# Optimization experiments

Hardware: AMD Instinct MI355X
Metric: run time of the kernel (lower is better)

## Reference

```python
import jax, jax.numpy as jnp
import numpy as np

D_MODEL, D_K, D_V, N_HEADS = 1024, 64, 64, 16


def setup_inputs() -> dict:
    key = jax.random.key(0)
    ks = jax.random.split(key, 8)
    B, S = 2, 2048
    s = 0.02
    return {
        "x": jax.random.normal(ks[0], (B, S, D_MODEL), dtype=jnp.float32),
        "Wq": jax.random.normal(ks[1], (D_MODEL, N_HEADS * D_K), dtype=jnp.float32) * s,
        "bq": jnp.zeros((N_HEADS * D_K,), dtype=jnp.float32),
        "Wk": jax.random.normal(ks[2], (D_MODEL, N_HEADS * D_K), dtype=jnp.float32) * s,
        "bk": jnp.zeros((N_HEADS * D_K,), dtype=jnp.float32),
        "Wv": jax.random.normal(ks[3], (D_MODEL, N_HEADS * D_V), dtype=jnp.float32) * s,
        "bv": jnp.zeros((N_HEADS * D_V,), dtype=jnp.float32),
        "Wo": jax.random.normal(ks[4], (N_HEADS * D_V, D_MODEL), dtype=jnp.float32) * s,
    }


def reference(x, Wq, bq, Wk, bk, Wv, bv, Wo):
    B, S, _ = x.shape
    split = lambda t, d: t.reshape(B, S, N_HEADS, d).transpose(0, 2, 1, 3)  # [B,H,S,d]
    Q = split(x @ Wq + bq, D_K)
    K = split(x @ Wk + bk, D_K)
    V = split(x @ Wv + bv, D_V)
    scores = jnp.einsum("bhqd,bhkd->bhqk", Q / jnp.sqrt(jnp.float32(D_K)), K)
    # causal mask: x + (1 - 1/tril) == 0 on allowed, -inf on disallowed
    causal = jnp.tril(jnp.ones((S, S), dtype=bool))
    scores = jnp.where(causal, scores, -jnp.inf)
    attn = jax.nn.softmax(scores, axis=-1)
    out = jnp.einsum("bhqk,bhkd->bhqd", attn, V)  # [B,H,S,d_v]
    out = out.transpose(0, 2, 1, 3).reshape(B, S, N_HEADS * D_V)
    return out @ Wo
```

## Files before the change

kernel.cpp:

```cpp
#include <hip/hip_runtime.h>
#include <hip/hip_bf16.h>
#include <hip/hip_fp16.h>
#include <cstdint>

#define DEVINL __device__ __forceinline__

typedef __attribute__((ext_vector_type(4))) float floatx4;
typedef __attribute__((ext_vector_type(8))) __bf16 bf16x8;
typedef __attribute__((ext_vector_type(4))) _Float16 half4;
typedef __attribute__((ext_vector_type(8))) _Float16 half8;
typedef __attribute__((ext_vector_type(4))) unsigned short u16x4;

DEVINL floatx4 mfma_16x16x32(bf16x8 a, bf16x8 b, floatx4 c) {
  return __builtin_amdgcn_mfma_f32_16x16x32_bf16(a, b, c, 0, 0, 0);
}
DEVINL floatx4 mfma_16x16x16_f16(half4 a, half4 b, floatx4 c) {
  return __builtin_amdgcn_mfma_f32_16x16x16f16(a, b, c, 0, 0, 0);
}

DEVINL void async_copy16(const void* g, void* l) {
  __builtin_amdgcn_global_load_lds(
      (__attribute__((address_space(1))) void*)(void*)g,
      (__attribute__((address_space(3))) void*)l, 16, 0, 0);
}

#define QSCALE 0.18033688011112042f

#define VS(d, s) \
  ((d) * 128 + (((((s) >> 3)) ^ ((d) & 7)) << 4) + ((s) & 7) * 2)

__global__ void cast_to_bf16(const float* __restrict__ in,
                             __hip_bfloat16* __restrict__ out, int n) {
  int i = (blockIdx.x * blockDim.x + threadIdx.x) * 4;
  if (i + 3 < n) {
    const float4 v = *(const float4*)&in[i];
    out[i + 0] = __float2bfloat16(v.x);
    out[i + 1] = __float2bfloat16(v.y);
    out[i + 2] = __float2bfloat16(v.z);
    out[i + 3] = __float2bfloat16(v.w);
  }
}

__global__ void transpose_cast4(const float* __restrict__ Wq,
                                const float* __restrict__ Wk,
                                const float* __restrict__ Wv,
                                const float* __restrict__ Wo,
                                __hip_bfloat16* __restrict__ Wt,
                                __hip_bfloat16* __restrict__ Wot) {
  __shared__ float tile[32][33];
  const int z = blockIdx.z;
  const float* W = (z == 0) ? Wq : (z == 1) ? Wk : (z == 2) ? Wv : Wo;
  __hip_bfloat16* dst = (z < 3) ? (Wt + ((int64_t)z << 20)) : Wot;
  const int k0 = blockIdx.x * 32, n0 = blockIdx.y * 32;
  const int tx = threadIdx.x, ty = threadIdx.y;
#pragma unroll
  for (int i = 0; i < 32; i += 8)
    tile[ty + i][tx] = W[(int64_t)(k0 + ty + i) * 1024 + n0 + tx];
  __syncthreads();
#pragma unroll
  for (int i = 0; i < 32; i += 8)
    dst[(int64_t)(n0 + ty + i) * 1024 + k0 + tx] =
        __float2bfloat16(tile[tx][ty + i]);
}

template <int MODE>
__global__ __launch_bounds__(256, 2) void gemm_bt(
    const __hip_bfloat16* __restrict__ A, const __hip_bfloat16* __restrict__ Bt,
    int M, int N, int K, const float* __restrict__ bq,
    const float* __restrict__ bk, const float* __restrict__ bv,
    __hip_bfloat16* __restrict__ Qb, __hip_bfloat16* __restrict__ Kb,
    _Float16* __restrict__ Vt, float* __restrict__ outf) {
  __shared__ __align__(16) __hip_bfloat16 As[128 * 32];
  __shared__ __align__(16) __hip_bfloat16 Bs[128 * 32];
  const int tid = threadIdx.x;
  const int wave = tid >> 6, lane = tid & 63;
  const int quad = lane >> 4, l16 = lane & 15;
  const int bm = blockIdx.x * 128, bn = blockIdx.y * 128;
  const int wm = (wave >> 1) * 64, wn = (wave & 1) * 64;

  floatx4 acc[4][4] = {};

  const int arow = tid >> 2, aseg = tid & 3;
  for (int k0 = 0; k0 < K; k0 += 32) {
#pragma unroll
    for (int i = 0; i < 2; ++i) {
      const int row = arow + i * 64;
      const int off = row * 32 + aseg * 8;
      async_copy16(A + (int64_t)(bm + row) * K + k0 + aseg * 8, As + off);
      async_copy16(Bt + (int64_t)(bn + row) * K + k0 + aseg * 8, Bs + off);
    }
    __syncthreads();
    bf16x8 af[4], bfr[4];
#pragma unroll
    for (int i = 0; i < 4; ++i) {
      af[i] = *(const bf16x8*)&As[(wm + i * 16 + l16) * 32 + quad * 8];
      bfr[i] = *(const bf16x8*)&Bs[(wn + i * 16 + l16) * 32 + quad * 8];
    }
#pragma unroll
    for (int i = 0; i < 4; ++i)
#pragma unroll
      for (int j = 0; j < 4; ++j)
        acc[i][j] = mfma_16x16x32(af[i], bfr[j], acc[i][j]);
    __syncthreads();
  }

  if (MODE == 1) {
#pragma unroll
    for (int i = 0; i < 4; ++i)
#pragma unroll
      for (int j = 0; j < 4; ++j) {
        const int n = bn + wn + j * 16 + l16;
#pragma unroll
        for (int r = 0; r < 4; ++r) {
          const int m = bm + wm + i * 16 + quad * 4 + r;
          outf[(int64_t)m * N + n] = acc[i][j][r];
        }
      }
  } else if (bn < 2048) {
#pragma unroll
    for (int i = 0; i < 4; ++i)
#pragma unroll
      for (int j = 0; j < 4; ++j) {
        const int n = bn + wn + j * 16 + l16;
        const int which = n >> 10, nn = n & 1023;
        const int h = nn >> 6, d = nn & 63;
        const float* bias = (which == 0) ? bq : bk;
#pragma unroll
        for (int r = 0; r < 4; ++r) {
          const int m = bm + wm + i * 16 + quad * 4 + r;
          const int b = m >> 11, s = m & 2047;
          float v = acc[i][j][r] + bias[nn];
          if (which == 0) v *= QSCALE;
          ((which == 0) ? Qb : Kb)[((int64_t)(b * 16 + h) * 2048 + s) * 64 + d] =
              __float2bfloat16(v);
        }
      }
  } else {
    char* scr = (wave & 1) ? (char*)Bs : (char*)As;
    const int h = ((bn + wn) & 1023) >> 6;
    const int bb = (bm + wm) >> 11;
    const int sbase = (bm + wm) & 2047;
    _Float16* dstV = Vt + (int64_t)(bb * 16 + h) * 64 * 2048;
#pragma unroll
    for (int phase = 0; phase < 2; ++phase) {
      __syncthreads();
      if ((wave >> 1) == phase) {
#pragma unroll
        for (int i = 0; i < 4; ++i)
#pragma unroll
          for (int j = 0; j < 4; ++j) {
            const int d = j * 16 + l16;
#pragma unroll
            for (int r = 0; r < 4; ++r) {
              const int s = i * 16 + quad * 4 + r;
              *(_Float16*)(scr + VS(d, s)) =
                  (_Float16)(acc[i][j][r] + bv[((bn + wn) & 1023) + d]);
            }
          }
      }
      __syncthreads();
      if ((wave >> 1) == phase) {
#pragma unroll
        for (int it = 0; it < 8; ++it) {
          const int idx = lane + it * 64;
          const int d = idx >> 3, sc = idx & 7;
          const half8 vv =
              *(const half8*)(scr + d * 128 + ((sc ^ (d & 7)) << 4));
          *(half8*)(dstV + (int64_t)d * 2048 + sbase + sc * 8) = vv;
        }
      }
    }
  }
}

__global__ __launch_bounds__(128, 2) void attn_kernel(
    const __hip_bfloat16* __restrict__ Qb, const __hip_bfloat16* __restrict__ Kb,
    const _Float16* __restrict__ Vt, __hip_bfloat16* __restrict__ Ab) {
  __shared__ __align__(16) char smem[32768];
  const int tid = threadIdx.x;
  const int wave = tid >> 6, lane = tid & 63;
  const int quad = lane >> 4, l16 = lane & 15;
  const int c = 31 - (int)(blockIdx.x >> 5);
  const int bh = blockIdx.x & 31;
  const int qbase = c * 64 + wave * 32;
  const int ktmax = c;

  const __hip_bfloat16* Qh = Qb + (int64_t)bh * 2048 * 64;
  const __hip_bfloat16* Kh = Kb + (int64_t)bh * 2048 * 64;
  const _Float16* Vh = Vt + (int64_t)bh * 64 * 2048;

  bf16x8 qf[2][2];
#pragma unroll
  for (int rt = 0; rt < 2; ++rt)
#pragma unroll
    for (int h = 0; h < 2; ++h)
      qf[rt][h] = *(const bf16x8*)&Qh[(int64_t)(qbase + rt * 16 + l16) * 64 +
                                      h * 32 + quad * 8];

  floatx4 o[2][4] = {};
  float lsum[2] = {0.f, 0.f};

  auto stage = [&](int buf, int k0s) {
#pragma unroll
    for (int i = 0; i < 4; ++i) {
      const int p = tid + i * 128;
      const int r = p >> 3, cc = (p & 7) ^ (r & 7);
      async_copy16(Kh + (int64_t)(k0s + r) * 64 + cc * 8,
                   smem + buf * 8192 + p * 16);
      async_copy16(Vh + (int64_t)r * 2048 + k0s + cc * 8,
                   smem + 16384 + buf * 8192 + p * 16);
    }
  };

  stage(0, 0);
  for (int kt = 0; kt <= ktmax; ++kt) {
    const int k0 = kt * 64;
    const int cur = kt & 1;
    __syncthreads();
    if (kt < ktmax) stage(cur ^ 1, k0 + 64);

    const char* kb = smem + cur * 8192;
    const char* vb = smem + 16384 + cur * 8192;
    const int sw = l16 & 7;

    bf16x8 kfr[4][2];
#pragma unroll
    for (int kk = 0; kk < 4; ++kk)
#pragma unroll
      for (int h = 0; h < 2; ++h)
        kfr[kk][h] = *(const bf16x8*)(kb + (kk * 16 + l16) * 128 +
                                      (((h * 4 + quad) ^ sw) << 4));

    floatx4 st[2][4];
#pragma unroll
    for (int kk = 0; kk < 4; ++kk)
#pragma unroll
      for (int rt = 0; rt < 2; ++rt) {
        floatx4 z = {};
        z = mfma_16x16x32(kfr[kk][0], qf[rt][0], z);
        st[rt][kk] = mfma_16x16x32(kfr[kk][1], qf[rt][1], z);
      }

    half4 vfr[4][4];
#pragma unroll
    for (int dt = 0; dt < 4; ++dt)
#pragma unroll
      for (int kk = 0; kk < 4; ++kk)
        vfr[dt][kk] = *(const half4*)(vb + (dt * 16 + l16) * 128 +
                                      (((kk * 2 + (quad >> 1)) ^ sw) << 4) +
                                      (quad & 1) * 8);

    const bool masked = (kt == ktmax);
    half4 pf[2][4];
#pragma unroll
    for (int rt = 0; rt < 2; ++rt) {
      const int qrow = qbase + rt * 16 + l16;
#pragma unroll
      for (int kk = 0; kk < 4; ++kk) {
#pragma unroll
        for (int r = 0; r < 4; ++r) {
          const int key = k0 + kk * 16 + quad * 4 + r;
          float p = __builtin_amdgcn_exp2f(st[rt][kk][r]);
          if (masked && key > qrow) p = 0.f;
          lsum[rt] += p;
          pf[rt][kk][r] = (_Float16)p;
        }
      }
    }

#pragma unroll
    for (int dt = 0; dt < 4; ++dt)
#pragma unroll
      for (int kk = 0; kk < 4; ++kk)
#pragma unroll
        for (int rt = 0; rt < 2; ++rt)
          o[rt][dt] = mfma_16x16x16_f16(vfr[dt][kk], pf[rt][kk], o[rt][dt]);
  }

#pragma unroll
  for (int rt = 0; rt < 2; ++rt) {
    lsum[rt] += __shfl_xor(lsum[rt], 16, 64);
    lsum[rt] += __shfl_xor(lsum[rt], 32, 64);
  }

  const int b = bh >> 4, h = bh & 15;
#pragma unroll
  for (int rt = 0; rt < 2; ++rt) {
    const float invl = 1.0f / lsum[rt];
#pragma unroll
    for (int dt = 0; dt < 4; ++dt) {
      u16x4 pack;
#pragma unroll
      for (int r = 0; r < 4; ++r)
        pack[r] = __builtin_bit_cast(unsigned short,
                                     __float2bfloat16(o[rt][dt][r] * invl));
      *(u16x4*)&Ab[(int64_t)(b * 2048 + qbase + rt * 16 + l16) * 1024 +
                   h * 64 + dt * 16 + quad * 4] = pack;
    }
  }
}

extern "C" void kernel_launch(void* const* d_in, const int* in_sizes, int n_in,
                              void* d_out, int out_size, void* d_ws,
                              size_t ws_size, hipStream_t stream) {
  const float* x = (const float*)d_in[0];
  const float* Wq = (const float*)d_in[1];
  const float* bq = (const float*)d_in[2];
  const float* Wk = (const float*)d_in[3];
  const float* bk = (const float*)d_in[4];
  const float* Wv = (const float*)d_in[5];
  const float* bv = (const float*)d_in[6];
  const float* Wo = (const float*)d_in[7];
  float* out = (float*)d_out;

  char* ws = (char*)d_ws;
  __hip_bfloat16* xb = (__hip_bfloat16*)(ws);
  __hip_bfloat16* Wt = (__hip_bfloat16*)(ws + (8ll << 20));
  __hip_bfloat16* Wot = (__hip_bfloat16*)(ws + (14ll << 20));
  __hip_bfloat16* Qb = (__hip_bfloat16*)(ws + (16ll << 20));
  __hip_bfloat16* Kb = (__hip_bfloat16*)(ws + (24ll << 20));
  _Float16* Vt = (_Float16*)(ws + (32ll << 20));
  __hip_bfloat16* Ab = xb;

  cast_to_bf16<<<4096, 256, 0, stream>>>(x, xb, 4096 * 1024);
  transpose_cast4<<<dim3(32, 32, 4), dim3(32, 8), 0, stream>>>(Wq, Wk, Wv, Wo,
                                                               Wt, Wot);
  gemm_bt<0><<<dim3(32, 24), 256, 0, stream>>>(xb, Wt, 4096, 3072, 1024, bq, bk,
                                               bv, Qb, Kb, Vt, nullptr);
  attn_kernel<<<dim3(1024), 128, 0, stream>>>(Qb, Kb, Vt, Ab);
  gemm_bt<1><<<dim3(32, 8), 256, 0, stream>>>(Ab, Wot, 4096, 1024, 1024,
                                              nullptr, nullptr, nullptr,
                                              nullptr, nullptr, nullptr, out);
}
```

Measured before the change: 182.8 us.

## Fuse prep kernels, widen GEMM K-step to 64 with swizzled LDS, retile output GEMM

```diff
diff --git a/kernel.cpp b/kernel.cpp
--- a/kernel.cpp
+++ b/kernel.cpp
@@ -29,30 +29,33 @@
 #define VS(d, s) \
   ((d) * 128 + (((((s) >> 3)) ^ ((d) & 7)) << 4) + ((s) & 7) * 2)
 
-__global__ void cast_to_bf16(const float* __restrict__ in,
-                             __hip_bfloat16* __restrict__ out, int n) {
-  int i = (blockIdx.x * blockDim.x + threadIdx.x) * 4;
-  if (i + 3 < n) {
-    const float4 v = *(const float4*)&in[i];
-    out[i + 0] = __float2bfloat16(v.x);
-    out[i + 1] = __float2bfloat16(v.y);
-    out[i + 2] = __float2bfloat16(v.z);
-    out[i + 3] = __float2bfloat16(v.w);
-  }
-}
-
-__global__ void transpose_cast4(const float* __restrict__ Wq,
-                                const float* __restrict__ Wk,
-                                const float* __restrict__ Wv,
-                                const float* __restrict__ Wo,
-                                __hip_bfloat16* __restrict__ Wt,
-                                __hip_bfloat16* __restrict__ Wot) {
+__global__ void prep(const float* __restrict__ x, const float* __restrict__ Wq,
+                     const float* __restrict__ Wk, const float* __restrict__ Wv,
+                     const float* __restrict__ Wo,
+                     __hip_bfloat16* __restrict__ xb,
+                     __hip_bfloat16* __restrict__ Wt,
+                     __hip_bfloat16* __restrict__ Wot) {
+  const int z = blockIdx.z;
+  const int tx = threadIdx.x, ty = threadIdx.y;
+  if (z == 4) {
+    const int bi = blockIdx.y * 32 + blockIdx.x;
+    const int tid = ty * 32 + tx;
+    const int base = bi * 4096 + tid * 4;
+#pragma unroll
+    for (int j = 0; j < 4; ++j) {
+      const int i = base + j * 1024;
+      const float4 v = *(const float4*)&x[i];
+      xb[i + 0] = __float2bfloat16(v.x);
+      xb[i + 1] = __float2bfloat16(v.y);
+      xb[i + 2] = __float2bfloat16(v.z);
+      xb[i + 3] = __float2bfloat16(v.w);
+    }
+    return;
+  }
   __shared__ float tile[32][33];
-  const int z = blockIdx.z;
   const float* W = (z == 0) ? Wq : (z == 1) ? Wk : (z == 2) ? Wv : Wo;
   __hip_bfloat16* dst = (z < 3) ? (Wt + ((int64_t)z << 20)) : Wot;
   const int k0 = blockIdx.x * 32, n0 = blockIdx.y * 32;
-  const int tx = threadIdx.x, ty = threadIdx.y;
 #pragma unroll
   for (int i = 0; i < 32; i += 8)
     tile[ty + i][tx] = W[(int64_t)(k0 + ty + i) * 1024 + n0 + tx];
@@ -63,52 +66,67 @@
         __float2bfloat16(tile[tx][ty + i]);
 }
 
-template <int MODE>
+template <int MODE, int TM, int TN>
 __global__ __launch_bounds__(256, 2) void gemm_bt(
     const __hip_bfloat16* __restrict__ A, const __hip_bfloat16* __restrict__ Bt,
     int M, int N, int K, const float* __restrict__ bq,
     const float* __restrict__ bk, const float* __restrict__ bv,
     __hip_bfloat16* __restrict__ Qb, __hip_bfloat16* __restrict__ Kb,
     _Float16* __restrict__ Vt, float* __restrict__ outf) {
-  __shared__ __align__(16) __hip_bfloat16 As[128 * 32];
-  __shared__ __align__(16) __hip_bfloat16 Bs[128 * 32];
+  constexpr int MI = TM / 32, NJ = TN / 32;
+  __shared__ __align__(16) char As[TM * 128];
+  __shared__ __align__(16) char Bs[TN * 128];
   const int tid = threadIdx.x;
   const int wave = tid >> 6, lane = tid & 63;
   const int quad = lane >> 4, l16 = lane & 15;
-  const int bm = blockIdx.x * 128, bn = blockIdx.y * 128;
-  const int wm = (wave >> 1) * 64, wn = (wave & 1) * 64;
-
-  floatx4 acc[4][4] = {};
-
-  const int arow = tid >> 2, aseg = tid & 3;
-  for (int k0 = 0; k0 < K; k0 += 32) {
-#pragma unroll
-    for (int i = 0; i < 2; ++i) {
-      const int row = arow + i * 64;
-      const int off = row * 32 + aseg * 8;
-      async_copy16(A + (int64_t)(bm + row) * K + k0 + aseg * 8, As + off);
-      async_copy16(Bt + (int64_t)(bn + row) * K + k0 + aseg * 8, Bs + off);
+  const int bm = blockIdx.x * TM, bn = blockIdx.y * TN;
+  const int wm = (wave >> 1) * (TM / 2), wn = (wave & 1) * (TN / 2);
+  const int sw = l16 & 7;
+
+  floatx4 acc[MI][NJ] = {};
+
+  for (int k0 = 0; k0 < K; k0 += 64) {
+#pragma unroll
+    for (int i = 0; i < TM / 32; ++i) {
+      const int p = tid + i * 256;
+      const int r = p >> 3, cc = (p & 7) ^ (r & 7);
+      async_copy16(A + (int64_t)(bm + r) * K + k0 + cc * 8, As + p * 16);
+    }
+#pragma unroll
+    for (int i = 0; i < TN / 32; ++i) {
+      const int p = tid + i * 256;
+      const int r = p >> 3, cc = (p & 7) ^ (r & 7);
+      async_copy16(Bt + (int64_t)(bn + r) * K + k0 + cc * 8, Bs + p * 16);
     }
     __syncthreads();
-    bf16x8 af[4], bfr[4];
-#pragma unroll
-    for (int i = 0; i < 4; ++i) {
-      af[i] = *(const bf16x8*)&As[(wm + i * 16 + l16) * 32 + quad * 8];
-      bfr[i] = *(const bf16x8*)&Bs[(wn + i * 16 + l16) * 32 + quad * 8];
-    }
-#pragma unroll
-    for (int i = 0; i < 4; ++i)
-#pragma unroll
-      for (int j = 0; j < 4; ++j)
-        acc[i][j] = mfma_16x16x32(af[i], bfr[j], acc[i][j]);
+    bf16x8 af[MI][2], bfr[NJ][2];
+#pragma unroll
+    for (int i = 0; i < MI; ++i)
+#pragma unroll
+      for (int h = 0; h < 2; ++h)
+        af[i][h] = *(const bf16x8*)(As + (wm + i * 16 + l16) * 128 +
+                                    (((h * 4 + quad) ^ sw) << 4));
+#pragma unroll
+    for (int j = 0; j < NJ; ++j)
+#pragma unroll
+      for (int h = 0; h < 2; ++h)
+        bfr[j][h] = *(const bf16x8*)(Bs + (wn + j * 16 + l16) * 128 +
+                                     (((h * 4 + quad) ^ sw) << 4));
+#pragma unroll
+    for (int i = 0; i < MI; ++i)
+#pragma unroll
+      for (int j = 0; j < NJ; ++j)
+#pragma unroll
+        for (int h = 0; h < 2; ++h)
+          acc[i][j] = mfma_16x16x32(af[i][h], bfr[j][h], acc[i][j]);
     __syncthreads();
   }
 
   if (MODE == 1) {
 #pragma unroll
-    for (int i = 0; i < 4; ++i)
-#pragma unroll
-      for (int j = 0; j < 4; ++j) {
+    for (int i = 0; i < MI; ++i)
+#pragma unroll
+      for (int j = 0; j < NJ; ++j) {
         const int n = bn + wn + j * 16 + l16;
 #pragma unroll
         for (int r = 0; r < 4; ++r) {
@@ -118,9 +136,9 @@
       }
   } else if (bn < 2048) {
 #pragma unroll
-    for (int i = 0; i < 4; ++i)
-#pragma unroll
-      for (int j = 0; j < 4; ++j) {
+    for (int i = 0; i < MI; ++i)
+#pragma unroll
+      for (int j = 0; j < NJ; ++j) {
         const int n = bn + wn + j * 16 + l16;
         const int which = n >> 10, nn = n & 1023;
         const int h = nn >> 6, d = nn & 63;
@@ -136,7 +154,7 @@
         }
       }
   } else {
-    char* scr = (wave & 1) ? (char*)Bs : (char*)As;
+    char* scr = (wave & 1) ? Bs : As;
     const int h = ((bn + wn) & 1023) >> 6;
     const int bb = (bm + wm) >> 11;
     const int sbase = (bm + wm) & 2047;
@@ -322,13 +340,12 @@
   _Float16* Vt = (_Float16*)(ws + (32ll << 20));
   __hip_bfloat16* Ab = xb;
 
-  cast_to_bf16<<<4096, 256, 0, stream>>>(x, xb, 4096 * 1024);
-  transpose_cast4<<<dim3(32, 32, 4), dim3(32, 8), 0, stream>>>(Wq, Wk, Wv, Wo,
-                                                               Wt, Wot);
-  gemm_bt<0><<<dim3(32, 24), 256, 0, stream>>>(xb, Wt, 4096, 3072, 1024, bq, bk,
-                                               bv, Qb, Kb, Vt, nullptr);
+  prep<<<dim3(32, 32, 5), dim3(32, 8), 0, stream>>>(x, Wq, Wk, Wv, Wo, xb, Wt,
+                                                    Wot);
+  gemm_bt<0, 128, 128><<<dim3(32, 24), 256, 0, stream>>>(
+      xb, Wt, 4096, 3072, 1024, bq, bk, bv, Qb, Kb, Vt, nullptr);
   attn_kernel<<<dim3(1024), 128, 0, stream>>>(Qb, Kb, Vt, Ab);
-  gemm_bt<1><<<dim3(32, 8), 256, 0, stream>>>(Ab, Wot, 4096, 1024, 1024,
-                                              nullptr, nullptr, nullptr,
-                                              nullptr, nullptr, nullptr, out);
-}
+  gemm_bt<1, 128, 64><<<dim3(32, 16), 256, 0, stream>>>(
+      Ab, Wot, 4096, 1024, 1024, nullptr, nullptr, nullptr, nullptr, nullptr,
+      nullptr, out);
+}
```

Result: faster. 168.0 us (-8.1%).
